# Kernel tuning notes

Hardware: AMD Instinct MI355X
Metric: run time of the kernel (lower is better)

## Reference

```python
import jax, jax.numpy as jnp
import numpy as np

B, N, C = 2, 6, 64
D_BINS, D_MIN, D_MAX = 64, 1.0, 60.0
IMG_H, IMG_W = 256, 704
FH, FW = 16, 44  # image_size / 16
BEV_H, BEV_W = 200, 200
XR = (-50.0, 50.0)
YR = (-50.0, 50.0)
BN_EPS = 1e-5


def create_frustum():
    # (D, FH, FW, 3) with last dim = (x_pix, y_pix, depth)
    ds = jnp.linspace(D_MIN, D_MAX, D_BINS)
    xs = jnp.linspace(0.0, IMG_W - 1.0, FW)
    ys = jnp.linspace(0.0, IMG_H - 1.0, FH)
    d, y, x = jnp.meshgrid(ds, ys, xs, indexing='ij')
    return jnp.stack([x, y, d], axis=-1)


def _conv(x, w, b, pad):
    y = jax.lax.conv_general_dilated(x, w, (1, 1), [(pad, pad), (pad, pad)],
                                     dimension_numbers=('NCHW', 'OIHW', 'NCHW'))
    return y + b[None, :, None, None]


def setup_inputs():
    key = jax.random.key(0)
    ks = jax.random.split(key, 4)
    features = jax.random.normal(ks[0], (B, N, C, FH, FW), jnp.float32)
    # realistic pinhole intrinsics
    fx = fy = 500.0
    K = jnp.array([[fx, 0.0, IMG_W / 2.0], [0.0, fy, IMG_H / 2.0], [0.0, 0.0, 1.0]], jnp.float32)
    intrinsics = jnp.broadcast_to(K, (B, N, 3, 3)).astype(jnp.float32)
    # cam2ego: yaw rotation per camera + small translation
    yaws = jnp.arange(N, dtype=jnp.float32) * (2.0 * np.pi / N)
    def ext(yaw):
        c, s = jnp.cos(yaw), jnp.sin(yaw)
        R = jnp.array([[c, -s, 0.0], [s, c, 0.0], [0.0, 0.0, 1.0]])
        return jnp.eye(4).at[:3, :3].set(R).at[:3, 3].set(jnp.array([1.0, 0.0, 1.5]))
    extrinsics = jnp.broadcast_to(jax.vmap(ext)(yaws), (B, N, 4, 4)).astype(jnp.float32)
    # DepthNet params: conv3x3(C->C) -> BN -> ReLU -> conv1x1(C->D)
    w1 = jax.random.normal(ks[1], (C, C, 3, 3), jnp.float32) * 0.05
    b1 = jnp.zeros((C,), jnp.float32)
    gamma = jnp.ones((C,), jnp.float32)
    beta = jnp.zeros((C,), jnp.float32)
    rmean = jnp.zeros((C,), jnp.float32)
    rvar = jnp.ones((C,), jnp.float32)
    w2 = jax.random.normal(ks[2], (D_BINS, C, 1, 1), jnp.float32) * 0.05
    b2 = jnp.zeros((D_BINS,), jnp.float32)
    return dict(features=features, intrinsics=intrinsics, extrinsics=extrinsics,
                w1=w1, b1=b1, gamma=gamma, beta=beta, rmean=rmean, rvar=rvar, w2=w2, b2=b2)


def reference(features, intrinsics, extrinsics, w1, b1, gamma, beta, rmean, rvar, w2, b2):
    feat = features.reshape(B * N, C, FH, FW)
    # DepthNet (BN in eval mode with running stats)
    h = _conv(feat, w1, b1, 1)
    h = (h - rmean[None, :, None, None]) * (gamma / jnp.sqrt(rvar + BN_EPS))[None, :, None, None] \
        + beta[None, :, None, None]
    h = jax.nn.relu(h)
    depth_logits = _conv(h, w2, b2, 0)                 # (BN, D, FH, FW)
    depth_probs = jax.nn.softmax(depth_logits, axis=1)
    # lift: outer product of features and depth distribution
    vol = feat[:, :, None] * depth_probs[:, None]      # (BN, C, D, FH, FW)
    vol = vol.reshape(B, N, C, D_BINS, FH, FW)

    frustum = create_frustum()                         # (D, FH, FW, 3)
    x, y, d = frustum[..., 0], frustum[..., 1], frustum[..., 2]
    pts = jnp.stack([x * d, y * d, d], axis=0).reshape(3, -1)   # (3, P), P = D*FH*FW
    Kinv = jnp.linalg.inv(intrinsics)                  # (B, N, 3, 3)
    cam = jnp.einsum('bnij,jp->bnip', Kinv, pts)       # camera-frame points
    R, t = extrinsics[..., :3, :3], extrinsics[..., :3, 3]
    ego = jnp.einsum('bnij,bnjp->bnip', R, cam) + t[..., None]  # (B, N, 3, P)

    resx = (XR[1] - XR[0]) / BEV_W
    resy = (YR[1] - YR[0]) / BEV_H
    ix = jnp.floor((ego[:, :, 0] - XR[0]) / resx).astype(jnp.int32)  # (B, N, P)
    iy = jnp.floor((ego[:, :, 1] - YR[0]) / resy).astype(jnp.int32)
    valid = (ix >= 0) & (ix < BEV_W) & (iy >= 0) & (iy < BEV_H)
    bidx = jnp.arange(B, dtype=jnp.int32)[:, None, None]
    idx = jnp.where(valid, bidx * (BEV_H * BEV_W) + iy * BEV_W + ix, 0)

    # splat: scatter-add depth-weighted features into the BEV grid
    vol_pts = vol.reshape(B, N, C, -1) * valid[:, :, None].astype(vol.dtype)
    vals = vol_pts.transpose(0, 1, 3, 2).reshape(-1, C)  # (B*N*P, C)
    bev = jax.ops.segment_sum(vals, idx.reshape(-1), num_segments=B * BEV_H * BEV_W)
    return bev.reshape(B, BEV_H, BEV_W, C).transpose(0, 3, 1, 2)  # (B, C, bevH, bevW)
```

## Files before the change

kernel.cpp:

```cpp
#include <hip/hip_runtime.h>
#include <math.h>

#define B_   2
#define N_   6
#define C_   64
#define D_   64
#define FH_  16
#define FW_  44
#define BN_  (B_*N_)
#define PIX_ (FH_*FW_)
#define NPIX (BN_*PIX_)
#define NPTS (BN_*D_*PIX_)
#define PPBN (D_*PIX_)
#define BEVH 200
#define BEVW 200
#define NCELL (BEVH*BEVW)
#define NBCELL (B_*NCELL)
#define NSCANB ((NBCELL + 255)/256)
#define PPW  64
#define GBLK (NPTS/(PPW*4))
#define NXCD 8
#define GCHUNK (GBLK/NXCD)
#define SCBLK (NPTS/256)

#define NB_ZOUT 5000
#define NB_ZSP  313
#define NB_TW   160
#define NB_PREP 1
#define NB_FT   132
#define NB_SETUP (NB_ZOUT + NB_ZSP + NB_TW + NB_PREP + NB_FT)

__global__ __launch_bounds__(256) void setup_kernel(
        const float* __restrict__ feat, const float* __restrict__ w1,
        const float* __restrict__ w2,
        const float* __restrict__ gamma, const float* __restrict__ beta,
        const float* __restrict__ rmean, const float* __restrict__ rvar,
        const float* __restrict__ intr,
        float* __restrict__ out, int* __restrict__ startp,
        float* __restrict__ w1t, float* __restrict__ w2t,
        float* __restrict__ bns, float* __restrict__ bnsh,
        float* __restrict__ kinv, float* __restrict__ feat_t) {
#pragma clang fp contract(off)
    __shared__ float lds[64][65];
    int blk = blockIdx.x;
    int t   = threadIdx.x;

    if (blk < NB_ZOUT) {
        ((float4*)out)[blk*256 + t] = float4{0.f, 0.f, 0.f, 0.f};
        return;
    }
    blk -= NB_ZOUT;
    if (blk < NB_ZSP) {
        int i = blk*256 + t;
        if (i < NBCELL + 1) startp[i] = 0;
        return;
    }
    blk -= NB_ZSP;
    if (blk < NB_TW) {
        int idx = blk*256 + t;
        if (idx < C_*C_*9) {
            int cout = idx / (C_*9);
            int r    = idx % (C_*9);
            int cin  = r / 9;
            int tap  = r % 9;
            w1t[(((cin >> 4)*9 + tap)*64 + cout)*16 + (cin & 15)] = w1[idx];
        } else if (idx < C_*C_*9 + D_*C_) {
            int j = idx - C_*C_*9;
            int d = j / C_, c = j % C_;
            w2t[c*D_ + d] = w2[j];
        }
        return;
    }
    blk -= NB_TW;
    if (blk < NB_PREP) {
        if (t < C_) {
            float s = gamma[t] / sqrtf(rvar[t] + 1e-5f);
            bns[t]  = s;
            bnsh[t] = beta[t] - rmean[t] * s;
        }
        if (t < BN_) {
            const float* K = intr + t*9;
            float A[3][3];
            for (int r = 0; r < 3; r++)
                for (int cc = 0; cc < 3; cc++) A[r][cc] = K[r*3 + cc];
            int ipiv[3];
            for (int j = 0; j < 3; j++) {
                int p = j; float mx = fabsf(A[j][j]);
                for (int i = j+1; i < 3; i++) {
                    float v = fabsf(A[i][j]);
                    if (v > mx) { mx = v; p = i; }
                }
                ipiv[j] = p;
                if (p != j)
                    for (int k = 0; k < 3; k++) { float tm = A[j][k]; A[j][k] = A[p][k]; A[p][k] = tm; }
                float rpiv = 1.0f / A[j][j];
                for (int i = j+1; i < 3; i++) A[i][j] = A[i][j] * rpiv;
                for (int k = j+1; k < 3; k++)
                    for (int i = j+1; i < 3; i++)
                        A[i][k] = A[i][k] - A[i][j] * A[j][k];
            }
            for (int j = 0; j < 3; j++) {
                float ajj = 1.0f / A[j][j];
                A[j][j] = ajj;
                float najj = -ajj;
                for (int jj = 0; jj < j; jj++) {
                    float temp = A[jj][j];
                    for (int i = 0; i < jj; i++) A[i][j] = A[i][j] + temp * A[i][jj];
                    A[jj][j] = A[jj][j] * A[jj][jj];
                }
                for (int i = 0; i < j; i++) A[i][j] = A[i][j] * najj;
            }
            for (int j = 1; j >= 0; j--) {
                float work[3];
                for (int i = j+1; i < 3; i++) { work[i] = A[i][j]; A[i][j] = 0.0f; }
                for (int k = j+1; k < 3; k++)
                    for (int i = 0; i < 3; i++)
                        A[i][j] = A[i][j] - A[i][k] * work[k];
            }
            for (int j = 2; j >= 0; j--) {
                int p = ipiv[j];
                if (p != j)
                    for (int i = 0; i < 3; i++) { float tm = A[i][j]; A[i][j] = A[i][p]; A[i][p] = tm; }
            }
            for (int k = 0; k < 9; k++) kinv[t*9 + k] = A[k/3][k%3];
        }
        return;
    }
    blk -= NB_PREP;
    {
        int bn   = blk / 11;
        int pb   = (blk % 11) * 64;
        int lane = t & 63;
        int r0   = t >> 6;
#pragma unroll
        for (int rr = 0; rr < 16; rr++) {
            int c = r0 + 4*rr;
            lds[c][lane] = feat[((size_t)bn*C_ + c)*PIX_ + pb + lane];
        }
        __syncthreads();
#pragma unroll
        for (int rr = 0; rr < 16; rr++) {
            int pr = r0 + 4*rr;
            feat_t[((size_t)bn*PIX_ + pb + pr)*C_ + lane] = lds[lane][pr];
        }
    }
}

__global__ __launch_bounds__(256) void enc_kernel(
        const float* __restrict__ feat_t,
        const float* __restrict__ w1t, const float* __restrict__ w2t,
        const float* __restrict__ bns, const float* __restrict__ bnsh,
        const float* __restrict__ b1,  const float* __restrict__ b2,
        float* __restrict__ probs) {
    __shared__ float wlds[9*C_*16];
    __shared__ float flds[36][C_];
    __shared__ float hl[16][C_];
    int blk = blockIdx.x;
    int bn  = blk / 44;
    int rem = blk % 44;
    int yt  = rem / 11;
    int xt  = rem % 11;
    int t   = threadIdx.x;
    int c   = t & 63;
    int w   = __builtin_amdgcn_readfirstlane(t >> 6);
    int y0  = yt*4;
    int x0  = xt*4;
    int y   = y0 + w;

    for (int s = w; s < 36; s += 4) {
        int srow = s / 6, scol = s % 6;
        int grow = y0 - 1 + srow;
        int gcol = x0 - 1 + scol;
        float v = 0.f;
        if (grow >= 0 && grow < FH_ && gcol >= 0 && gcol < FW_)
            v = feat_t[((size_t)bn*PIX_ + grow*FW_ + gcol)*C_ + c];
        flds[s][c] = v;
    }

    float h0 = b1[c], h1 = h0, h2 = h0, h3 = h0;

    for (int cc16 = 0; cc16 < 4; cc16++) {
        __syncthreads();
        {
            const float4* s4 = (const float4*)(w1t + cc16*(9*C_*16));
            float4* d4 = (float4*)wlds;
#pragma unroll
            for (int i = 0; i < 9; i++)
                d4[t + 256*i] = s4[t + 256*i];
        }
        __syncthreads();
        int cc = cc16*16;
#pragma unroll
        for (int cg = 0; cg < 16; cg += 4) {
            float4 wv4[9];
#pragma unroll
            for (int tap = 0; tap < 9; tap++)
                wv4[tap] = *(const float4*)&wlds[(tap*64 + c)*16 + cg];
            float4 fr4[3][6];
#pragma unroll
            for (int r = 0; r < 3; r++)
#pragma unroll
                for (int cl = 0; cl < 6; cl++)
                    fr4[r][cl] = *(const float4*)&flds[(w + r)*6 + cl][cc + cg];
#pragma unroll
            for (int k = 0; k < 4; k++) {
#pragma unroll
                for (int ky = 0; ky < 3; ky++) {
#pragma unroll
                    for (int kx = 0; kx < 3; kx++) {
                        float wv = ((const float*)&wv4[ky*3 + kx])[k];
                        h0 = fmaf(wv, ((const float*)&fr4[ky][kx + 0])[k], h0);
                        h1 = fmaf(wv, ((const float*)&fr4[ky][kx + 1])[k], h1);
                        h2 = fmaf(wv, ((const float*)&fr4[ky][kx + 2])[k], h2);
                        h3 = fmaf(wv, ((const float*)&fr4[ky][kx + 3])[k], h3);
                    }
                }
            }
        }
    }

    float sc = bns[c], sh = bnsh[c];
    {
        float v0 = fmaf(h0, sc, sh); hl[w*4 + 0][c] = v0 > 0.f ? v0 : 0.f;
        float v1 = fmaf(h1, sc, sh); hl[w*4 + 1][c] = v1 > 0.f ? v1 : 0.f;
        float v2 = fmaf(h2, sc, sh); hl[w*4 + 2][c] = v2 > 0.f ? v2 : 0.f;
        float v3 = fmaf(h3, sc, sh); hl[w*4 + 3][c] = v3 > 0.f ? v3 : 0.f;
    }
    __syncthreads();

    float l0 = b2[c], l1 = l0, l2 = l0, l3 = l0;
    for (int c2 = 0; c2 < C_; c2++) {
        float wv = w2t[c2*D_ + c];
        l0 = fmaf(wv, hl[w*4 + 0][c2], l0);
        l1 = fmaf(wv, hl[w*4 + 1][c2], l1);
        l2 = fmaf(wv, hl[w*4 + 2][c2], l2);
        l3 = fmaf(wv, hl[w*4 + 3][c2], l3);
    }

    float lv[4] = {l0, l1, l2, l3};
#pragma unroll
    for (int p = 0; p < 4; p++) {
        float l = lv[p];
        float m = l;
        for (int off = 32; off; off >>= 1) m = fmaxf(m, __shfl_xor(m, off));
        float e = expf(l - m);
        float s = e;
        for (int off = 32; off; off >>= 1) s += __shfl_xor(s, off);
        probs[((size_t)bn*PIX_ + y*FW_ + x0 + p)*D_ + c] = e / s;
    }
}

__device__ __forceinline__ int compute_cell(int i, const float* __restrict__ kinv,
                                            const float* __restrict__ ext) {
#pragma clang fp contract(off)
    int x  = i % FW_;
    int y  = (i / FW_) % FH_;
    int d  = (i / PIX_) % D_;
    int bn = i / PPBN;

    const float* kv = kinv + bn*9;
    const float* e  = ext  + bn*16;

    float u  = (x == FW_-1) ? 703.0f : (float)((double)x * (703.0/43.0));
    float vv = (float)((double)y * 17.0);
    float dd = (d == D_-1) ? 60.0f  : (float)(1.0 + (double)d * (59.0/63.0));

    float px = u * dd;
    float py = vv * dd;
    float pz = dd;

    float cx = (kv[0]*px + kv[1]*py) + kv[2]*pz;
    float cy = (kv[3]*px + kv[4]*py) + kv[5]*pz;
    float cz = (kv[6]*px + kv[7]*py) + kv[8]*pz;

    float ex = (e[0]*cx + e[1]*cy) + e[2]*cz;
    float ey = (e[4]*cx + e[5]*cy) + e[6]*cz;
    ex = ex + e[3];
    ey = ey + e[7];

    float gx = (ex + 50.0f) / 0.5f;
    float gy = (ey + 50.0f) / 0.5f;
    int ix = (int)floorf(gx);
    int iy = (int)floorf(gy);
    return (ix >= 0 && ix < BEVW && iy >= 0 && iy < BEVH) ? (iy*BEVW + ix) : -1;
}

__device__ __forceinline__ void run_info(int fc, int lane,
                                         bool& isLeader, int& runLen, int& lead) {
    int prev = __shfl_up(fc, 1);
    isLeader = (lane == 0) || (fc != prev);
    unsigned long long mask = __ballot(isLeader);
    unsigned long long hi = (lane == 63) ? 0ull : (mask >> (lane + 1));
    int next = hi ? (lane + 1 + __builtin_ctzll(hi)) : 64;
    runLen = next - lane;
    unsigned long long lo = mask & (~0ull >> (63 - lane));
    lead = 63 - __builtin_clzll(lo);
}

__global__ __launch_bounds__(256) void geomhist_kernel(
        const float* __restrict__ ext, const float* __restrict__ kinv,
        int* __restrict__ counts) {
    int i = blockIdx.x * 256 + threadIdx.x;
    int lane = threadIdx.x & 63;
    int fc = -1;
    if (i < NPTS) {
        int cell = compute_cell(i, kinv, ext);
        if (cell >= 0) fc = (i / (PPBN * N_)) * NCELL + cell;
    }
    bool isLeader; int runLen, lead;
    run_info(fc, lane, isLeader, runLen, lead);
    if (isLeader && fc >= 0) atomicAdd(&counts[fc], runLen);
}

__global__ __launch_bounds__(256) void scanA_kernel(
        int* __restrict__ startp, int* __restrict__ cursor, int* __restrict__ bsum) {
    __shared__ int sdata[256];
    int t = threadIdx.x;
    int i = blockIdx.x * 256 + t;
    int v = (i < NBCELL) ? startp[1 + i] : 0;
    sdata[t] = v;
    __syncthreads();
#pragma unroll
    for (int off = 1; off < 256; off <<= 1) {
        int add = (t >= off) ? sdata[t - off] : 0;
        __syncthreads();
        sdata[t] += add;
        __syncthreads();
    }
    if (i < NBCELL) {
        startp[1 + i] = sdata[t];
        cursor[i]     = sdata[t] - v;
    }
    if (t == 255) bsum[blockIdx.x] = sdata[255];
}

__global__ __launch_bounds__(512) void scanC_kernel(
        int* __restrict__ startp, int* __restrict__ cursor,
        const int* __restrict__ bsum) {
    __shared__ int sdata[512];
    int t = threadIdx.x;
    int v = (t < NSCANB) ? bsum[t] : 0;
    sdata[t] = v;
    __syncthreads();
#pragma unroll
    for (int off = 1; off < 512; off <<= 1) {
        int add = (t >= off) ? sdata[t - off] : 0;
        __syncthreads();
        sdata[t] += add;
        __syncthreads();
    }
    int i = blockIdx.x * 512 + t;
    if (i >= NBCELL) return;
    int j = i >> 8;
    int off = (j == 0) ? 0 : sdata[j - 1];
    startp[1 + i] += off;
    cursor[i]     += off;
}

__global__ __launch_bounds__(256) void geomscatter_kernel(
        const float* __restrict__ ext, const float* __restrict__ kinv,
        const float* __restrict__ probs,
        int* __restrict__ cursor, int2* __restrict__ plist2) {
    int blk = (blockIdx.x % NXCD) * (SCBLK/NXCD) + blockIdx.x / NXCD;
    int i = blk * 256 + threadIdx.x;
    int lane = threadIdx.x & 63;
    int fc = -1, pixg = 0;
    float pr = 0.f;
    if (i < NPTS) {
        int cell = compute_cell(i, kinv, ext);
        if (cell >= 0) {
            int pix = i % PIX_;
            int d   = (i / PIX_) % D_;
            int bn  = i / PPBN;
            fc   = (bn / N_) * NCELL + cell;
            pixg = bn*PIX_ + pix;
            pr   = probs[(size_t)pixg*D_ + d];
        }
    }
    bool isLeader; int runLen, lead;
    run_info(fc, lane, isLeader, runLen, lead);
    int base = 0;
    if (isLeader && fc >= 0) base = atomicAdd(&cursor[fc], runLen);
    base = __shfl(base, lead);
    if (fc >= 0)
        plist2[base + (lane - lead)] = make_int2(__float_as_int(pr),
                                                 pixg | (fc << 14));
}

__device__ __forceinline__ float cell_accum(
        const int2* __restrict__ plist2, const float* __restrict__ feat_t,
        int q0, int q1, int lane) {
    float a0 = 0.f, a1 = 0.f, a2 = 0.f, a3 = 0.f;
    int q = q0;
    for (; q + 4 <= q1; q += 4) {
        int2 r0 = plist2[q];
        int2 r1 = plist2[q + 1];
        int2 r2 = plist2[q + 2];
        int2 r3 = plist2[q + 3];
        float f0 = feat_t[(size_t)(r0.y & 0x3FFF)*C_ + lane];
        float f1 = feat_t[(size_t)(r1.y & 0x3FFF)*C_ + lane];
        float f2 = feat_t[(size_t)(r2.y & 0x3FFF)*C_ + lane];
        float f3 = feat_t[(size_t)(r3.y & 0x3FFF)*C_ + lane];
        a0 = fmaf(__int_as_float(r0.x), f0, a0);
        a1 = fmaf(__int_as_float(r1.x), f1, a1);
        a2 = fmaf(__int_as_float(r2.x), f2, a2);
        a3 = fmaf(__int_as_float(r3.x), f3, a3);
    }
    for (; q < q1; q++) {
        int2 r = plist2[q];
        a0 = fmaf(__int_as_float(r.x),
                  feat_t[(size_t)(r.y & 0x3FFF)*C_ + lane], a0);
    }
    return (a0 + a1) + (a2 + a3);
}

__global__ __launch_bounds__(256) void gather4_kernel(
        const float* __restrict__ feat_t, const int* __restrict__ startp,
        const int2* __restrict__ plist2, float* __restrict__ out) {
    int blk  = (blockIdx.x % NXCD) * GCHUNK + blockIdx.x / NXCD;
    int gid  = blk * 256 + threadIdx.x;
    int W    = gid >> 6;
    int lane = gid & 63;
    int total = startp[NBCELL];
    int p0 = W * PPW;
    if (p0 >= total) return;
    int pe = min(p0 + PPW, total);
    int p  = p0;

    {
        int2 r = plist2[p0];
        int fc = ((unsigned)r.y) >> 14;
        int cs = startp[fc], ce = startp[fc + 1];
        if (cs < p0) {
            if (ce - cs > 2*PPW) {
                float acc = cell_accum(plist2, feat_t, p0, min(pe, ce), lane);
                int bb   = fc >= NCELL;
                int cell = fc - bb*NCELL;
                atomicAdd(out + ((size_t)(bb*C_ + lane))*NCELL + cell, acc);
            }
            p = ce;
        }
    }
    while (p < pe) {
        int2 r = plist2[p];
        int fc = ((unsigned)r.y) >> 14;
        int ce = startp[fc + 1];
        bool big = (ce - p > 2*PPW);
        int b2 = big ? min(ce, pe) : ce;
        float acc = cell_accum(plist2, feat_t, p, b2, lane);
        int bb   = fc >= NCELL;
        int cell = fc - bb*NCELL;
        float* addr = out + ((size_t)(bb*C_ + lane))*NCELL + cell;
        if (big) atomicAdd(addr, acc);
        else     *addr = acc;
        p = ce;
    }
}

extern "C" void kernel_launch(void* const* d_in, const int* in_sizes, int n_in,
                              void* d_out, int out_size, void* d_ws, size_t ws_size,
                              hipStream_t stream) {
    const float* feat  = (const float*)d_in[0];
    const float* intr  = (const float*)d_in[1];
    const float* ext   = (const float*)d_in[2];
    const float* w1    = (const float*)d_in[3];
    const float* b1    = (const float*)d_in[4];
    const float* gamma = (const float*)d_in[5];
    const float* beta  = (const float*)d_in[6];
    const float* rmean = (const float*)d_in[7];
    const float* rvar  = (const float*)d_in[8];
    const float* w2    = (const float*)d_in[9];
    const float* b2    = (const float*)d_in[10];
    float* out = (float*)d_out;
    (void)in_sizes; (void)n_in; (void)out_size; (void)ws_size;

    int2*  plist2 = (int2*)d_ws;
    float* w1t    = (float*)(plist2 + NPTS);
    float* w2t    = w1t + C_*C_*9;
    float* bns    = w2t + D_*C_;
    float* bnsh   = bns + C_;
    float* kinv   = bnsh + C_;
    float* probs  = kinv + BN_*9;
    float* feat_t = probs + NPTS;
    int*   startp = (int*)(feat_t + NPTS);
    int*   cursor = startp + (NBCELL + 1);
    int*   bsum   = cursor + NBCELL;

    setup_kernel<<<NB_SETUP, 256, 0, stream>>>(feat, w1, w2, gamma, beta,
                                               rmean, rvar, intr, out, startp,
                                               w1t, w2t, bns, bnsh, kinv, feat_t);
    enc_kernel<<<528, 256, 0, stream>>>(feat_t, w1t, w2t, bns, bnsh, b1, b2, probs);
    geomhist_kernel<<<NPTS/256, 256, 0, stream>>>(ext, kinv, startp + 1);
    scanA_kernel<<<NSCANB, 256, 0, stream>>>(startp, cursor, bsum);
    scanC_kernel<<<(NBCELL + 511)/512, 512, 0, stream>>>(startp, cursor, bsum);
    geomscatter_kernel<<<SCBLK, 256, 0, stream>>>(ext, kinv, probs, cursor, plist2);
    gather4_kernel<<<GBLK, 256, 0, stream>>>(feat_t, startp, plist2, out);
}
```

Before: 188.6 us.

## Stage gather output in cell-major layout and transpose to NCHW afterward

The gather kernel now writes each cell's 64 channels contiguously into a workspace buffer in cell-major order, so stores are coalesced across lanes instead of strided by the cell count in NCHW. A separate LDS-tiled transpose kernel then converts this staging buffer into the required (B, C, H, W) output. The zeroing pass targets the staging buffer instead of the output. This adds a full extra read and write of the output plus one more launch, and falls back to the old direct path when the workspace is too small.

```diff
diff --git a/kernel.cpp b/kernel.cpp
--- a/kernel.cpp
+++ b/kernel.cpp
@@ -36,7 +36,7 @@
         const float* __restrict__ gamma, const float* __restrict__ beta,
         const float* __restrict__ rmean, const float* __restrict__ rvar,
         const float* __restrict__ intr,
-        float* __restrict__ out, int* __restrict__ startp,
+        float* __restrict__ zt, int* __restrict__ startp,
         float* __restrict__ w1t, float* __restrict__ w2t,
         float* __restrict__ bns, float* __restrict__ bnsh,
         float* __restrict__ kinv, float* __restrict__ feat_t) {
@@ -46,7 +46,7 @@
     int t   = threadIdx.x;
 
     if (blk < NB_ZOUT) {
-        ((float4*)out)[blk*256 + t] = float4{0.f, 0.f, 0.f, 0.f};
+        ((float4*)zt)[blk*256 + t] = float4{0.f, 0.f, 0.f, 0.f};
         return;
     }
     blk -= NB_ZOUT;
@@ -414,7 +414,69 @@
     return (a0 + a1) + (a2 + a3);
 }
 
-__global__ __launch_bounds__(256) void gather4_kernel(
+__global__ __launch_bounds__(256) void gather4s_kernel(
+        const float* __restrict__ feat_t, const int* __restrict__ startp,
+        const int2* __restrict__ plist2, float* __restrict__ out_t) {
+    int blk  = (blockIdx.x % NXCD) * GCHUNK + blockIdx.x / NXCD;
+    int gid  = blk * 256 + threadIdx.x;
+    int W    = gid >> 6;
+    int lane = gid & 63;
+    int total = startp[NBCELL];
+    int p0 = W * PPW;
+    if (p0 >= total) return;
+    int pe = min(p0 + PPW, total);
+    int p  = p0;
+
+    {
+        int2 r = plist2[p0];
+        int fc = ((unsigned)r.y) >> 14;
+        int cs = startp[fc], ce = startp[fc + 1];
+        if (cs < p0) {
+            if (ce - cs > 2*PPW) {
+                float acc = cell_accum(plist2, feat_t, p0, min(pe, ce), lane);
+                atomicAdd(out_t + (size_t)fc*C_ + lane, acc);
+            }
+            p = ce;
+        }
+    }
+    while (p < pe) {
+        int2 r = plist2[p];
+        int fc = ((unsigned)r.y) >> 14;
+        int ce = startp[fc + 1];
+        bool big = (ce - p > 2*PPW);
+        int b2 = big ? min(ce, pe) : ce;
+        float acc = cell_accum(plist2, feat_t, p, b2, lane);
+        float* addr = out_t + (size_t)fc*C_ + lane;
+        if (big) atomicAdd(addr, acc);
+        else     *addr = acc;
+        p = ce;
+    }
+}
+
+__global__ __launch_bounds__(256) void transT_kernel(
+        const float* __restrict__ out_t, float* __restrict__ out) {
+    __shared__ float lds[64][65];
+    int blk   = blockIdx.x;
+    int b     = blk / (NCELL/64);
+    int cell0 = (blk % (NCELL/64)) * 64;
+    int t     = threadIdx.x;
+    int lane  = t & 63;
+    int r0    = t >> 6;
+    size_t fcb = (size_t)b*NCELL + cell0;
+#pragma unroll
+    for (int k = 0; k < 16; k++) {
+        int r = r0 + 4*k;
+        lds[r][lane] = out_t[(fcb + r)*C_ + lane];
+    }
+    __syncthreads();
+#pragma unroll
+    for (int k = 0; k < 16; k++) {
+        int ch = r0 + 4*k;
+        out[((size_t)(b*C_ + ch))*NCELL + cell0 + lane] = lds[lane][ch];
+    }
+}
+
+__global__ __launch_bounds__(256) void gather4d_kernel(
         const float* __restrict__ feat_t, const int* __restrict__ startp,
         const int2* __restrict__ plist2, float* __restrict__ out) {
     int blk  = (blockIdx.x % NXCD) * GCHUNK + blockIdx.x / NXCD;
@@ -472,7 +534,7 @@
     const float* w2    = (const float*)d_in[9];
     const float* b2    = (const float*)d_in[10];
     float* out = (float*)d_out;
-    (void)in_sizes; (void)n_in; (void)out_size; (void)ws_size;
+    (void)in_sizes; (void)n_in; (void)out_size;
 
     int2*  plist2 = (int2*)d_ws;
     float* w1t    = (float*)(plist2 + NPTS);
@@ -485,14 +547,24 @@
     int*   startp = (int*)(feat_t + NPTS);
     int*   cursor = startp + (NBCELL + 1);
     int*   bsum   = cursor + NBCELL;
+    float* out_t  = (float*)(bsum + NSCANB);
+    size_t need   = (size_t)((char*)(out_t + (size_t)NBCELL*C_) - (char*)d_ws);
+    bool staged   = (ws_size >= need);
+
+    float* zt = staged ? out_t : out;
 
     setup_kernel<<<NB_SETUP, 256, 0, stream>>>(feat, w1, w2, gamma, beta,
-                                               rmean, rvar, intr, out, startp,
+                                               rmean, rvar, intr, zt, startp,
                                                w1t, w2t, bns, bnsh, kinv, feat_t);
     enc_kernel<<<528, 256, 0, stream>>>(feat_t, w1t, w2t, bns, bnsh, b1, b2, probs);
     geomhist_kernel<<<NPTS/256, 256, 0, stream>>>(ext, kinv, startp + 1);
     scanA_kernel<<<NSCANB, 256, 0, stream>>>(startp, cursor, bsum);
     scanC_kernel<<<(NBCELL + 511)/512, 512, 0, stream>>>(startp, cursor, bsum);
     geomscatter_kernel<<<SCBLK, 256, 0, stream>>>(ext, kinv, probs, cursor, plist2);
-    gather4_kernel<<<GBLK, 256, 0, stream>>>(feat_t, startp, plist2, out);
-}
+    if (staged) {
+        gather4s_kernel<<<GBLK, 256, 0, stream>>>(feat_t, startp, plist2, out_t);
+        transT_kernel<<<NBCELL/64, 256, 0, stream>>>(out_t, out);
+    } else {
+        gather4d_kernel<<<GBLK, 256, 0, stream>>>(feat_t, startp, plist2, out);
+    }
+}
```

Measured after the change: 184.8 us. 1.02x faster.
